# Performance work log

Hardware: AMD Instinct MI355X
Metric: run time of the kernel (lower is better)

The kernel has to match this reference:

```python
import jax, jax.numpy as jnp
import numpy as np

K = 3
STRIDE = 1
PAD = 1


def _unfold(x, k, stride, pad):
    # x: (B, C, H, W) -> (B, C*k*k, L) matching torch.nn.functional.unfold
    # ordering: channel slowest, then kh, then kw.
    B, C, H, W = x.shape
    Hout = (H + 2 * pad - k) // stride + 1
    Wout = (W + 2 * pad - k) // stride + 1
    xp = jnp.pad(x, ((0, 0), (0, 0), (pad, pad), (pad, pad)))
    patches = []  # fixed k*k loop (9 iters), not a data-dim loop
    for i in range(k):
        for j in range(k):
            patches.append(xp[:, :, i:i + stride * Hout:stride, j:j + stride * Wout:stride])
    # (B, C, k*k, Hout, Wout) -> (B, C*k*k, L)
    p = jnp.stack(patches, axis=2)
    return p.reshape(B, C * k * k, Hout * Wout), Hout, Wout


def setup_inputs() -> dict:
    key = jax.random.key(0)
    k1, k2 = jax.random.split(key)
    x = jax.random.normal(k1, (4, 32, 56, 56), dtype=jnp.float32)
    weights = jax.random.normal(k2, (64, 32, 3, 3), dtype=jnp.float32)
    return {"x": x, "weights": weights}


def reference(x, weights):
    B = x.shape[0]
    O = weights.shape[0]
    mu_w = jnp.mean(jnp.abs(weights))
    x_unf, Hout, Wout = _unfold(x, K, STRIDE, PAD)      # (B, Ckk, L)
    w_unf = weights.reshape(O, -1)                        # (O, Ckk)
    # min-plus 'convolution': broadcast min then reduce over patch dim
    min_val = jnp.minimum(x_unf[:, None, :, :], w_unf[None, :, :, None])  # (B, O, Ckk, L)
    z = mu_w * jnp.sum(min_val, axis=2)                   # (B, O, L)
    return z.reshape(B, O, Hout, Wout)
```

## Files before the change

### kernel.cpp

```cpp
#include <hip/hip_runtime.h>

#define CIN  32
#define OCH  64
#define HH   56
#define WW   56
#define BB   4
#define OT   4
#define IMG  (HH * WW)
#define NW   18432
#define PH   58
#define PW   58
#define PIMG (PH * PW)
#define NXPK (BB * (CIN/2) * PIMG)
#define XPKBLKS (NXPK / 256)
#define NWPK (OCH * (CIN/2) * 9)
#define WPKBLKS (NWPK / 256)
#define WOFFu 64
#define XOFFu (WOFFu + NWPK)

typedef _Float16 h2 __attribute__((ext_vector_type(2)));

static __device__ __forceinline__ h2 pkmin_vv(h2 xv, unsigned wu) {
    unsigned xu = __builtin_bit_cast(unsigned, xv);
    unsigned ru;
    asm("v_pk_min_f16 %0, %1, %2" : "=v"(ru) : "v"(xu), "v"(wu));
    return __builtin_bit_cast(h2, ru);
}

__global__ __launch_bounds__(256) void prep(const float* __restrict__ x,
                                            const float* __restrict__ w,
                                            float* __restrict__ ws) {
    unsigned* wsu = reinterpret_cast<unsigned*>(ws);
    if (blockIdx.x < XPKBLKS) {
        int idx = blockIdx.x * 256 + threadIdx.x;
        int bc  = idx / PIMG;
        int r   = idx - bc * PIMG;
        int ph  = r / PW;
        int pw  = r - ph * PW;
        int hh  = ph - 1, wc = pw - 1;
        float v0 = 0.f, v1 = 0.f;
        if ((unsigned)hh < (unsigned)HH && (unsigned)wc < (unsigned)WW) {
            int base = ((bc >> 4) * CIN + (bc & 15) * 2) * IMG + hh * WW + wc;
            v0 = x[base];
            v1 = x[base + IMG];
        }
        h2 p; p.x = (_Float16)v0; p.y = (_Float16)v1;
        wsu[XOFFu + idx] = __builtin_bit_cast(unsigned, p);
        return;
    }
    if (blockIdx.x < XPKBLKS + WPKBLKS) {
        int idx = (blockIdx.x - XPKBLKS) * 256 + threadIdx.x;
        int otile = idx / 576;
        int r     = idx - otile * 576;
        int wvq   = r / 288;
        int r2    = r - wvq * 288;
        int oo    = r2 / 72;
        int r3    = r2 - oo * 72;
        int cl    = r3 / 9;
        int t     = r3 - cl * 9;
        int o     = otile * OT + oo;
        int cp    = wvq * 8 + cl;
        int src   = o * (CIN * 9) + cp * 18 + t;
        h2 p; p.x = (_Float16)w[src]; p.y = (_Float16)w[src + 9];
        wsu[WOFFu + idx] = __builtin_bit_cast(unsigned, p);
        return;
    }
    float s = 0.f;
    const float4* w4 = reinterpret_cast<const float4*>(w);
    #pragma unroll
    for (int k = 0; k < 18; ++k) {
        float4 v = w4[k * 256 + threadIdx.x];
        s += fabsf(v.x) + fabsf(v.y) + fabsf(v.z) + fabsf(v.w);
    }
    #pragma unroll
    for (int off = 32; off; off >>= 1) s += __shfl_down(s, off);
    __shared__ float sm[4];
    if ((threadIdx.x & 63) == 0) sm[threadIdx.x >> 6] = s;
    __syncthreads();
    if (threadIdx.x == 0)
        ws[0] = (sm[0] + sm[1] + sm[2] + sm[3]) * (1.0f / (float)NW);
}

__global__ __launch_bounds__(128) void minconv_kernel(const float* __restrict__ ws,
                                                      const float* __restrict__ wts,
                                                      float* __restrict__ out) {
    const unsigned* wsu = reinterpret_cast<const unsigned*>(ws);
    const int lane = threadIdx.x & 63;
    const int wv   = threadIdx.x >> 6;
    const int wvs  = __builtin_amdgcn_readfirstlane(wv);
    const int hw = blockIdx.x * 64 + lane;
    const int o0 = blockIdx.y * OT;
    const int b  = blockIdx.z;
    const int h  = hw / WW;
    const int w  = hw - h * WW;

    const float mu = ws[0];

    __shared__ unsigned wlds[576];
    __shared__ float red[2][2][64];

    {
        const unsigned* wt = wsu + WOFFu + blockIdx.y * 576;
        const int tid = threadIdx.x;
        *reinterpret_cast<uint4*>(&wlds[tid * 4]) =
            *reinterpret_cast<const uint4*>(&wt[tid * 4]);
        if (tid < 64) wlds[512 + tid] = wt[512 + tid];
    }

    const int cp0 = wvs * 8;
    const unsigned* xq = wsu + XOFFu + (size_t)(b * 16 + cp0) * PIMG + h * PW + w;
    h2 xall[72];
    #pragma unroll
    for (int cp = 0; cp < 8; ++cp)
        #pragma unroll
        for (int kh = 0; kh < 3; ++kh)
            #pragma unroll
            for (int kw = 0; kw < 3; ++kw)
                xall[cp * 9 + kh * 3 + kw] =
                    __builtin_bit_cast(h2, xq[cp * PIMG + kh * PW + kw]);

    __syncthreads();

    h2 ones; ones.x = (_Float16)1.f; ones.y = (_Float16)1.f;
    float acc0 = 0.f, acc1 = 0.f, acc2 = 0.f, acc3 = 0.f;
    const unsigned* wl = wlds + wv * 288;

    #pragma unroll
    for (int oo = 0; oo < OT; ++oo) {
        float ae = 0.f, ao = 0.f;
        #pragma unroll
        for (int k = 0; k < 18; ++k) {
            uint4 q = *reinterpret_cast<const uint4*>(&wl[oo * 72 + k * 4]);
            h2 m0 = pkmin_vv(xall[k * 4 + 0], q.x);
            ae = __builtin_amdgcn_fdot2(m0, ones, ae, false);
            h2 m1 = pkmin_vv(xall[k * 4 + 1], q.y);
            ao = __builtin_amdgcn_fdot2(m1, ones, ao, false);
            h2 m2 = pkmin_vv(xall[k * 4 + 2], q.z);
            ae = __builtin_amdgcn_fdot2(m2, ones, ae, false);
            h2 m3 = pkmin_vv(xall[k * 4 + 3], q.w);
            ao = __builtin_amdgcn_fdot2(m3, ones, ao, false);
        }
        float a = ae + ao;
        switch (oo) {
            case 0: acc0 = a; break;
            case 1: acc1 = a; break;
            case 2: acc2 = a; break;
            case 3: acc3 = a; break;
        }
    }

    if (wv == 0) {
        red[0][0][lane] = acc2;
        red[0][1][lane] = acc3;
    } else {
        red[1][0][lane] = acc0;
        red[1][1][lane] = acc1;
    }
    __syncthreads();

    float* ob = out + ((size_t)b * OCH + o0) * IMG + hw;
    if (wv == 0) {
        ob[0]       = mu * (acc0 + red[1][0][lane]);
        ob[IMG]     = mu * (acc1 + red[1][1][lane]);
    } else {
        ob[2 * IMG] = mu * (acc2 + red[0][0][lane]);
        ob[3 * IMG] = mu * (acc3 + red[0][1][lane]);
    }
}

extern "C" void kernel_launch(void* const* d_in, const int* in_sizes, int n_in,
                              void* d_out, int out_size, void* d_ws, size_t ws_size,
                              hipStream_t stream) {
    const float* x   = (const float*)d_in[0];
    const float* w   = (const float*)d_in[1];
    float*       out = (float*)d_out;
    float*       ws  = (float*)d_ws;

    prep<<<XPKBLKS + WPKBLKS + 1, 256, 0, stream>>>(x, w, ws);
    dim3 grid(IMG / 64, OCH / OT, BB);
    minconv_kernel<<<grid, 128, 0, stream>>>(ws, w, out);
}
```

Before: 69.30 us.

## Process two batches per block and reorder packed weights for output-tile reuse

Each block now covers two batch images (b and b+2), and the grid's batch dimension is halved. The inner loop now runs over channel pairs instead of output channels, so each LDS weight load (uint4 holding 4 output channels per tap) is reused across 4 outputs and 2 batches. The weight packing order changes to match. Input loads are streamed per channel pair instead of preloaded into 72 registers, which cuts register pressure but leaves fewer blocks in the grid.

Measured after the change: 70.05 us. About the same (+1.1%).

```diff
diff --git a/kernel.cpp b/kernel.cpp
--- a/kernel.cpp
+++ b/kernel.cpp
@@ -54,10 +54,10 @@
         int r     = idx - otile * 576;
         int wvq   = r / 288;
         int r2    = r - wvq * 288;
-        int oo    = r2 / 72;
-        int r3    = r2 - oo * 72;
-        int cl    = r3 / 9;
-        int t     = r3 - cl * 9;
+        int cl    = r2 / 36;
+        int r3    = r2 - cl * 36;
+        int t     = r3 >> 2;
+        int oo    = r3 & 3;
         int o     = otile * OT + oo;
         int cp    = wvq * 8 + cl;
         int src   = o * (CIN * 9) + cp * 18 + t;
@@ -90,14 +90,14 @@
     const int wvs  = __builtin_amdgcn_readfirstlane(wv);
     const int hw = blockIdx.x * 64 + lane;
     const int o0 = blockIdx.y * OT;
-    const int b  = blockIdx.z;
+    const int b2 = blockIdx.z;
     const int h  = hw / WW;
     const int w  = hw - h * WW;
 
     const float mu = ws[0];
 
-    __shared__ unsigned wlds[576];
-    __shared__ float red[2][2][64];
+    __shared__ __align__(16) unsigned wlds[576];
+    __shared__ float red[2][4][64];
 
     {
         const unsigned* wt = wsu + WOFFu + blockIdx.y * 576;
@@ -108,63 +108,73 @@
     }
 
     const int cp0 = wvs * 8;
-    const unsigned* xq = wsu + XOFFu + (size_t)(b * 16 + cp0) * PIMG + h * PW + w;
-    h2 xall[72];
-    #pragma unroll
-    for (int cp = 0; cp < 8; ++cp)
-        #pragma unroll
-        for (int kh = 0; kh < 3; ++kh)
-            #pragma unroll
-            for (int kw = 0; kw < 3; ++kw)
-                xall[cp * 9 + kh * 3 + kw] =
-                    __builtin_bit_cast(h2, xq[cp * PIMG + kh * PW + kw]);
+    const unsigned* xqA = wsu + XOFFu + (size_t)(b2 * 16 + cp0) * PIMG + h * PW + w;
+    const unsigned* xqB = xqA + 2 * 16 * PIMG;
 
     __syncthreads();
 
     h2 ones; ones.x = (_Float16)1.f; ones.y = (_Float16)1.f;
-    float acc0 = 0.f, acc1 = 0.f, acc2 = 0.f, acc3 = 0.f;
+    float aA0 = 0.f, aA1 = 0.f, aA2 = 0.f, aA3 = 0.f;
+    float aB0 = 0.f, aB1 = 0.f, aB2 = 0.f, aB3 = 0.f;
     const unsigned* wl = wlds + wv * 288;
 
     #pragma unroll
-    for (int oo = 0; oo < OT; ++oo) {
-        float ae = 0.f, ao = 0.f;
+    for (int cp = 0; cp < 8; ++cp) {
+        h2 xA[9], xB[9];
         #pragma unroll
-        for (int k = 0; k < 18; ++k) {
-            uint4 q = *reinterpret_cast<const uint4*>(&wl[oo * 72 + k * 4]);
-            h2 m0 = pkmin_vv(xall[k * 4 + 0], q.x);
-            ae = __builtin_amdgcn_fdot2(m0, ones, ae, false);
-            h2 m1 = pkmin_vv(xall[k * 4 + 1], q.y);
-            ao = __builtin_amdgcn_fdot2(m1, ones, ao, false);
-            h2 m2 = pkmin_vv(xall[k * 4 + 2], q.z);
-            ae = __builtin_amdgcn_fdot2(m2, ones, ae, false);
-            h2 m3 = pkmin_vv(xall[k * 4 + 3], q.w);
-            ao = __builtin_amdgcn_fdot2(m3, ones, ao, false);
-        }
-        float a = ae + ao;
-        switch (oo) {
-            case 0: acc0 = a; break;
-            case 1: acc1 = a; break;
-            case 2: acc2 = a; break;
-            case 3: acc3 = a; break;
+        for (int kh = 0; kh < 3; ++kh)
+            #pragma unroll
+            for (int kw = 0; kw < 3; ++kw) {
+                xA[kh * 3 + kw] = __builtin_bit_cast(h2, xqA[cp * PIMG + kh * PW + kw]);
+                xB[kh * 3 + kw] = __builtin_bit_cast(h2, xqB[cp * PIMG + kh * PW + kw]);
+            }
+        #pragma unroll
+        for (int t = 0; t < 9; ++t) {
+            uint4 q = *reinterpret_cast<const uint4*>(&wl[cp * 36 + t * 4]);
+            h2 mA0 = pkmin_vv(xA[t], q.x);
+            aA0 = __builtin_amdgcn_fdot2(mA0, ones, aA0, false);
+            h2 mA1 = pkmin_vv(xA[t], q.y);
+            aA1 = __builtin_amdgcn_fdot2(mA1, ones, aA1, false);
+            h2 mA2 = pkmin_vv(xA[t], q.z);
+            aA2 = __builtin_amdgcn_fdot2(mA2, ones, aA2, false);
+            h2 mA3 = pkmin_vv(xA[t], q.w);
+            aA3 = __builtin_amdgcn_fdot2(mA3, ones, aA3, false);
+            h2 mB0 = pkmin_vv(xB[t], q.x);
+            aB0 = __builtin_amdgcn_fdot2(mB0, ones, aB0, false);
+            h2 mB1 = pkmin_vv(xB[t], q.y);
+            aB1 = __builtin_amdgcn_fdot2(mB1, ones, aB1, false);
+            h2 mB2 = pkmin_vv(xB[t], q.z);
+            aB2 = __builtin_amdgcn_fdot2(mB2, ones, aB2, false);
+            h2 mB3 = pkmin_vv(xB[t], q.w);
+            aB3 = __builtin_amdgcn_fdot2(mB3, ones, aB3, false);
         }
     }
 
     if (wv == 0) {
-        red[0][0][lane] = acc2;
-        red[0][1][lane] = acc3;
+        red[0][0][lane] = aB0;
+        red[0][1][lane] = aB1;
+        red[0][2][lane] = aB2;
+        red[0][3][lane] = aB3;
     } else {
-        red[1][0][lane] = acc0;
-        red[1][1][lane] = acc1;
+        red[1][0][lane] = aA0;
+        red[1][1][lane] = aA1;
+        red[1][2][lane] = aA2;
+        red[1][3][lane] = aA3;
     }
     __syncthreads();
 
-    float* ob = out + ((size_t)b * OCH + o0) * IMG + hw;
     if (wv == 0) {
-        ob[0]       = mu * (acc0 + red[1][0][lane]);
-        ob[IMG]     = mu * (acc1 + red[1][1][lane]);
+        float* ob = out + ((size_t)b2 * OCH + o0) * IMG + hw;
+        ob[0 * IMG] = mu * (aA0 + red[1][0][lane]);
+        ob[1 * IMG] = mu * (aA1 + red[1][1][lane]);
+        ob[2 * IMG] = mu * (aA2 + red[1][2][lane]);
+        ob[3 * IMG] = mu * (aA3 + red[1][3][lane]);
     } else {
-        ob[2 * IMG] = mu * (acc2 + red[0][0][lane]);
-        ob[3 * IMG] = mu * (acc3 + red[0][1][lane]);
+        float* ob = out + ((size_t)(b2 + 2) * OCH + o0) * IMG + hw;
+        ob[0 * IMG] = mu * (aB0 + red[0][0][lane]);
+        ob[1 * IMG] = mu * (aB1 + red[0][1][lane]);
+        ob[2 * IMG] = mu * (aB2 + red[0][2][lane]);
+        ob[3 * IMG] = mu * (aB3 + red[0][3][lane]);
     }
 }
 
@@ -177,6 +187,6 @@
     float*       ws  = (float*)d_ws;
 
     prep<<<XPKBLKS + WPKBLKS + 1, 256, 0, stream>>>(x, w, ws);
-    dim3 grid(IMG / 64, OCH / OT, BB);
+    dim3 grid(IMG / 64, OCH / OT, BB / 2);
     minconv_kernel<<<grid, 128, 0, stream>>>(ws, w, out);
 }
```
